# Optimization experiments

Hardware: AMD Instinct MI355X
Metric: run time of the kernel (lower is better)

## Reference

```python
import jax, jax.numpy as jnp
import numpy as np
from jax import lax

EPS = 1e-5
SLOPE = 0.01  # LeakyReLU negative slope
MAX_DISP = 5
KSIZE = 3  # correlation patch kernel size


def conv_bn_lrelu(x, w, b, g, be, stride=1):
    # x: (B, Cin, L), w: (Cout, Cin, K)
    k = w.shape[-1]
    pad = (k - 1) // 2
    y = lax.conv_general_dilated(x, w, (stride,), [(pad, pad)],
                                 dimension_numbers=('NCH', 'OIH', 'NCH'))
    y = y + b[None, :, None]
    # BatchNorm1d in training mode: biased batch stats over (B, L)
    m = y.mean(axis=(0, 2), keepdims=True)
    v = y.var(axis=(0, 2), keepdims=True)
    y = g[None, :, None] * (y - m) * lax.rsqrt(v + EPS) + be[None, :, None]
    return jnp.where(y >= 0, y, SLOPE * y)


def upsample_nearest(x, size):
    # F.interpolate(mode='nearest'): idx = floor(i * L_in / L_out)
    L = x.shape[-1]
    idx = (jnp.arange(size) * L) // size
    return x[:, :, idx]


def fusion(f1, f2, K=KSIZE, D=MAX_DISP):
    # Banded correlation: corr[b, d, i] = <patch1[b,:,i], patch2[b,:,clamp(i+d)]>
    # where patches stack K clamped neighbors along the channel dim.
    B, C, N = f1.shape
    h = K // 2
    win = jnp.clip(jnp.arange(N)[:, None] + jnp.arange(-h, h + 1)[None, :], 0, N - 1)  # (N, K)
    p1 = f1[:, :, win].transpose(0, 1, 3, 2).reshape(B, C * K, N)
    p2 = f2[:, :, win].transpose(0, 1, 3, 2).reshape(B, C * K, N)
    pts = jnp.arange(N)
    bands = []
    for d in range(-D, D + 1):  # small fixed loop over 2D+1 = 11 displacements
        j = jnp.clip(pts + d, 0, N - 1)
        bands.append(jnp.sum(p1 * p2[:, :, j], axis=1))  # (B, N)
    return jnp.stack(bands, axis=1)  # (B, 2D+1, N)


def _make_block(key, cin, cout, k):
    kw, _ = jax.random.split(key)
    scale = np.sqrt(2.0 / (1.0 + 0.1 ** 2) / (cin * k)).astype(np.float32)
    w = jax.random.normal(kw, (cout, cin, k), dtype=jnp.float32) * scale
    b = jnp.zeros((cout,), jnp.float32)
    g = jnp.ones((cout,), jnp.float32)
    be = jnp.zeros((cout,), jnp.float32)
    return w, b, g, be


def setup_inputs() -> dict:
    key = jax.random.key(0)
    ks = jax.random.split(key, 8)
    B, N, CIN = 8, 16384, 1
    scan1 = jax.random.normal(ks[0], (B, N, CIN), dtype=jnp.float32)
    inp = {'scan1': scan1}
    specs = [('enc0', CIN, 64, 3), ('enc1', 64, 128, 3), ('enc2', 128, 256, 3),
             ('dec1', 2 * MAX_DISP + 1 + 128, 128, 3), ('dec0', 128 + 64, 128, 3),
             ('flow', 128 + CIN, 2, 1)]
    for i, (name, cin, cout, k) in enumerate(specs):
        w, b, g, be = _make_block(ks[i + 1], cin, cout, k)
        inp[name + '_w'] = w
        inp[name + '_b'] = b
        inp[name + '_g'] = g
        inp[name + '_be'] = be
    return inp


def reference(scan1,
              enc0_w, enc0_b, enc0_g, enc0_be,
              enc1_w, enc1_b, enc1_g, enc1_be,
              enc2_w, enc2_b, enc2_g, enc2_be,
              dec1_w, dec1_b, dec1_g, dec1_be,
              dec0_w, dec0_b, dec0_g, dec0_be,
              flow_w, flow_b, flow_g, flow_be):
    x1 = scan1.transpose(0, 2, 1)  # (B, Cin, N)
    # scan2 defaults to scan1, so feat2_* == feat1_* (identical BN batch stats)
    f0 = conv_bn_lrelu(x1, enc0_w, enc0_b, enc0_g, enc0_be, stride=2)
    f1 = conv_bn_lrelu(f0, enc1_w, enc1_b, enc1_g, enc1_be, stride=2)
    f2 = conv_bn_lrelu(f1, enc2_w, enc2_b, enc2_g, enc2_be, stride=2)
    feat = fusion(f2, f2)  # (B, 11, N/8)
    up1 = upsample_nearest(feat, f1.shape[-1])
    up1 = jnp.concatenate((f1, up1), axis=1)
    up1 = conv_bn_lrelu(up1, dec1_w, dec1_b, dec1_g, dec1_be, stride=1)
    up0 = upsample_nearest(up1, f0.shape[-1])
    up0 = jnp.concatenate((f0, up0), axis=1)
    up0 = conv_bn_lrelu(up0, dec0_w, dec0_b, dec0_g, dec0_be, stride=1)
    out = upsample_nearest(up0, x1.shape[-1])
    out = jnp.concatenate((x1, out), axis=1)
    out = conv_bn_lrelu(out, flow_w, flow_b, flow_g, flow_be, stride=1)
    return out.transpose(0, 2, 1)  # (B, N, 2)
```

## Files before the change

kernel.cpp:

```cpp
#include <hip/hip_runtime.h>
#include <cstddef>

#define SLOPE 0.01f
#define BN_EPS 1e-5f

typedef __attribute__((ext_vector_type(8))) short short8;
typedef __attribute__((ext_vector_type(4))) float floatx4;

__device__ __forceinline__ float lrelu(float t) { return fmaxf(t, SLOPE * t); }

__device__ __forceinline__ unsigned short f2bf(float f) {
    union { float f; unsigned int u; } x; x.f = f;
    unsigned int r = (x.u + 0x7fff + ((x.u >> 16) & 1)) >> 16;
    return (unsigned short)r;
}
__device__ __forceinline__ float bf2f(unsigned short h) {
    union { unsigned int u; float f; } x; x.u = ((unsigned int)h) << 16;
    return x.f;
}

__device__ __forceinline__ void bn_coeff(const float* __restrict__ st,
                                         const float* __restrict__ g,
                                         const float* __restrict__ be,
                                         float invN, int c, float& sc, float& sh) {
    float m   = st[c] * invN;
    float var = fmaf(st[256 + c], invN, -m * m);
    float r   = rsqrtf(var + BN_EPS);
    sc = g[c] * r;
    sh = fmaf(-sc, m, be[c]);
}

__device__ __forceinline__ void reorder1(const float* __restrict__ w,
                                         unsigned short* __restrict__ wr,
                                         int Cout, int Cinpad, int Cin, int id) {
    int ci = id % Cinpad;
    int rest = id / Cinpad;
    int co = rest % Cout;
    int t  = rest / Cout;
    float v = (ci < Cin) ? w[((size_t)co * Cin + ci) * 3 + t] : 0.0f;
    wr[id] = f2bf(v);
}

__global__ __launch_bounds__(256) void prepw_all_kernel(
    const float* __restrict__ w1, unsigned short* __restrict__ o1,
    const float* __restrict__ w2, unsigned short* __restrict__ o2,
    const float* __restrict__ w3, unsigned short* __restrict__ o3,
    const float* __restrict__ w4, unsigned short* __restrict__ o4)
{
    int id = blockIdx.x * 256 + threadIdx.x;
    const int n1 = 3 * 128 * 64;
    const int n2 = 3 * 256 * 128;
    const int n3 = 3 * 128 * 160;
    const int n4 = 3 * 128 * 192;
    if (id < n1) { reorder1(w1, o1, 128, 64, 64, id); return; }
    id -= n1;
    if (id < n2) { reorder1(w2, o2, 256, 128, 128, id); return; }
    id -= n2;
    if (id < n3) { reorder1(w3, o3, 128, 160, 139, id); return; }
    id -= n3;
    if (id < n4) { reorder1(w4, o4, 128, 192, 192, id); return; }
}

__global__ __launch_bounds__(256) void enc0_kernel(
    const float* __restrict__ x, const float* __restrict__ w,
    const float* __restrict__ bias, unsigned short* __restrict__ f0,
    float* __restrict__ st)
{
    __shared__ float ssum[64], ssq[64];
    const int tid = threadIdx.x;
    const int co  = tid & 63;
    const int b   = blockIdx.z;
    if (tid < 64) { ssum[tid] = 0.f; ssq[tid] = 0.f; }
    __syncthreads();
    const float w0 = w[co * 3], w1 = w[co * 3 + 1], w2 = w[co * 3 + 2];
    const float bs = bias[co];
    const float* xb = x + (size_t)b * 16384;
    float lsum = 0.f, lsq = 0.f;
    const int obase = blockIdx.x * 128 + (tid >> 6) * 32;
    for (int k = 0; k < 32; ++k) {
        int o = obase + k;
        int xi = 2 * o - 1;
        float x0v = (xi >= 0) ? xb[xi] : 0.f;
        float a = bs;
        a = fmaf(w0, x0v, a);
        a = fmaf(w1, xb[xi + 1], a);
        a = fmaf(w2, xb[xi + 2], a);
        f0[((size_t)(b * 8192 + o)) * 64 + co] = f2bf(a);
        lsum += a; lsq = fmaf(a, a, lsq);
    }
    atomicAdd(&ssum[co], lsum);
    atomicAdd(&ssq[co], lsq);
    __syncthreads();
    if (tid < 64) {
        atomicAdd(&st[tid],       ssum[tid]);
        atomicAdd(&st[256 + tid], ssq[tid]);
    }
}

template<int STRIDE>
__global__ __launch_bounds__(256) void conv_mfma_kernel(
    const unsigned short* __restrict__ xA, int CAc,
    const float* __restrict__ stA, const float* __restrict__ gA,
    const float* __restrict__ beA, float invNA,
    const unsigned short* __restrict__ xB, int CBc,
    const float* __restrict__ stB, const float* __restrict__ gB,
    const float* __restrict__ beB, float invNB,
    const unsigned short* __restrict__ Wr, const float* __restrict__ bias,
    unsigned short* __restrict__ out, int L_in, int L_out, int Cout,
    float* __restrict__ st)
{
    constexpr int SEG = 127 * STRIDE + 3;
    __shared__ __align__(16) unsigned short x_tile[2][SEG * 32];
    __shared__ float ssum[64], ssq[64];
    __shared__ float csc[192], csh[192];

    const int tid  = threadIdx.x;
    const int wv   = tid >> 6;
    const int lane = tid & 63;
    const int col  = lane & 15;
    const int quad = lane >> 4;
    const int oblk = blockIdx.x * 128;
    const int cob  = blockIdx.y * 64;
    const int b    = blockIdx.z;
    const int nch    = CAc + CBc;
    const int CApad  = CAc * 32;
    const int CBpad  = CBc * 32;
    const int Cinpad = nch * 32;
    const int LB     = L_in >> 1;
    const bool nA = (stA != nullptr);
    const bool nB = (stB != nullptr);

    if (tid < 64) { ssum[tid] = 0.f; ssq[tid] = 0.f; }
    for (int c = tid; c < Cinpad; c += 256) {
        float sc = 1.f, sh = 0.f;
        if (c < CApad) { if (nA) bn_coeff(stA, gA, beA, invNA, c, sc, sh); }
        else           { if (nB) bn_coeff(stB, gB, beB, invNB, c - CApad, sc, sh); }
        csc[c] = sc; csh[c] = sh;
    }

    floatx4 acc[2][4];
    #pragma unroll
    for (int ps = 0; ps < 2; ++ps)
        #pragma unroll
        for (int s = 0; s < 4; ++s)
            acc[ps][s] = (floatx4){0.f, 0.f, 0.f, 0.f};

    const int x0 = oblk * STRIDE - 1;

    auto stage = [&](int ch, int buf) {
        const bool applyN = (ch < CAc) ? nA : nB;
        for (int r = tid; r < SEG * 4; r += 256) {
            const int pi = r >> 2, part = r & 3;
            const int gp = x0 + pi;
            short8 v = {0, 0, 0, 0, 0, 0, 0, 0};
            if (gp >= 0 && gp < L_in) {
                if (ch < CAc)
                    v = *(const short8*)(xA + ((size_t)b * L_in + gp) * CApad + ch * 32 + part * 8);
                else
                    v = *(const short8*)(xB + ((size_t)b * LB + (gp >> 1)) * CBpad + (ch - CAc) * 32 + part * 8);
                if (applyN) {
                    const int cb = ch * 32 + part * 8;
                    #pragma unroll
                    for (int e = 0; e < 8; ++e) {
                        float f = bf2f((unsigned short)v[e]);
                        f = lrelu(fmaf(f, csc[cb + e], csh[cb + e]));
                        v[e] = (short)f2bf(f);
                    }
                }
            }
            *(short8*)(x_tile[buf] + (size_t)r * 8) = v;
        }
    };

    __syncthreads();
    stage(0, 0);
    __syncthreads();

    for (int ch = 0; ch < nch; ++ch) {
        const int cur = ch & 1;
        if (ch + 1 < nch) stage(ch + 1, cur ^ 1);

        #pragma unroll
        for (int t = 0; t < 3; ++t) {
            short8 bfr[4];
            #pragma unroll
            for (int s = 0; s < 4; ++s)
                bfr[s] = *(const short8*)(Wr +
                    ((size_t)(t * Cout + cob + s * 16 + col)) * Cinpad + ch * 32 + quad * 8);
            #pragma unroll
            for (int ps = 0; ps < 2; ++ps) {
                const int xi = (wv * 32 + ps * 16 + col) * STRIDE + t;
                short8 afr = *(const short8*)(x_tile[cur] + xi * 32 + quad * 8);
                #pragma unroll
                for (int s = 0; s < 4; ++s)
                    acc[ps][s] = __builtin_amdgcn_mfma_f32_16x16x32_bf16(afr, bfr[s], acc[ps][s], 0, 0, 0);
            }
        }
        __syncthreads();
    }

    float bv[4];
    #pragma unroll
    for (int s = 0; s < 4; ++s) bv[s] = bias[cob + s * 16 + col];
    #pragma unroll
    for (int ps = 0; ps < 2; ++ps)
        #pragma unroll
        for (int s = 0; s < 4; ++s)
            #pragma unroll
            for (int r = 0; r < 4; ++r)
                acc[ps][s][r] += bv[s];

    #pragma unroll
    for (int ps = 0; ps < 2; ++ps) {
        const int pos0 = oblk + wv * 32 + ps * 16 + quad * 4;
        #pragma unroll
        for (int s = 0; s < 4; ++s) {
            unsigned short* op = out + ((size_t)b * L_out + pos0) * Cout + cob + s * 16 + col;
            #pragma unroll
            for (int r = 0; r < 4; ++r)
                op[(size_t)r * Cout] = f2bf(acc[ps][s][r]);
        }
    }

    #pragma unroll
    for (int s = 0; s < 4; ++s) {
        float v = 0.f, q = 0.f;
        #pragma unroll
        for (int ps = 0; ps < 2; ++ps)
            #pragma unroll
            for (int r = 0; r < 4; ++r) {
                float a = acc[ps][s][r];
                v += a; q = fmaf(a, a, q);
            }
        v += __shfl_xor(v, 16); v += __shfl_xor(v, 32);
        q += __shfl_xor(q, 16); q += __shfl_xor(q, 32);
        if (quad == 0) {
            atomicAdd(&ssum[s * 16 + col], v);
            atomicAdd(&ssq[s * 16 + col],  q);
        }
    }
    __syncthreads();
    if (tid < 64) {
        atomicAdd(&st[cob + tid],       ssum[tid]);
        atomicAdd(&st[256 + cob + tid], ssq[tid]);
    }
}

__global__ __launch_bounds__(256) void fusion_kernel(
    const unsigned short* __restrict__ f2,
    const float* __restrict__ st, const float* __restrict__ g,
    const float* __restrict__ be, float invN,
    unsigned short* __restrict__ feat)
{
    constexpr int ROWS = 44;
    constexpr int CPAD = 272;
    __shared__ __align__(16) unsigned short tile[ROWS * CPAD];
    __shared__ float csc[256], csh[256];
    const int tid = threadIdx.x;
    const int p0  = blockIdx.x * 32;
    const int b   = blockIdx.y;
    const unsigned short* base = f2 + (size_t)b * 2048 * 256;

    {
        float sc, sh;
        bn_coeff(st, g, be, invN, tid, sc, sh);
        csc[tid] = sc; csh[tid] = sh;
    }
    __syncthreads();
    float scr[8], shr[8];
    {
        const int cb = (tid & 31) * 8;
        #pragma unroll
        for (int e = 0; e < 8; ++e) { scr[e] = csc[cb + e]; shr[e] = csh[cb + e]; }
    }
    for (int r = tid; r < ROWS * 32; r += 256) {
        int row = r >> 5, piece = r & 31;
        int grow = min(max(p0 - 6 + row, 0), 2047);
        short8 v = *(const short8*)(base + (size_t)grow * 256 + piece * 8);
        #pragma unroll
        for (int e = 0; e < 8; ++e) {
            float f = bf2f((unsigned short)v[e]);
            f = lrelu(fmaf(f, scr[e], shr[e]));
            v[e] = (short)f2bf(f);
        }
        *(short8*)(tile + row * CPAD + piece * 8) = v;
    }
    __syncthreads();

    const int il = tid >> 3;
    const int q  = tid & 7;
    const int i  = p0 + il;

    float acc[11];
    #pragma unroll
    for (int d = 0; d < 11; ++d) acc[d] = 0.f;

    int ra[3];
    #pragma unroll
    for (int j = 0; j < 3; ++j)
        ra[j] = (min(max(i + j - 1, 0), 2047) - p0 + 6) * CPAD;
    int rb[11][3];
    #pragma unroll
    for (int d = 0; d < 11; ++d) {
        int i2 = min(max(i + d - 5, 0), 2047);
        #pragma unroll
        for (int j = 0; j < 3; ++j)
            rb[d][j] = (min(max(i2 + j - 1, 0), 2047) - p0 + 6) * CPAD;
    }

    for (int ck = 0; ck < 4; ++ck) {
        const int coff = q * 32 + ck * 8;
        float fa[3][8];
        #pragma unroll
        for (int j = 0; j < 3; ++j) {
            short8 v = *(const short8*)(tile + ra[j] + coff);
            #pragma unroll
            for (int e = 0; e < 8; ++e) fa[j][e] = bf2f((unsigned short)v[e]);
        }
        #pragma unroll
        for (int d = 0; d < 11; ++d) {
            #pragma unroll
            for (int j = 0; j < 3; ++j) {
                short8 v = *(const short8*)(tile + rb[d][j] + coff);
                #pragma unroll
                for (int e = 0; e < 8; ++e)
                    acc[d] = fmaf(fa[j][e], bf2f((unsigned short)v[e]), acc[d]);
            }
        }
    }

    #pragma unroll
    for (int d = 0; d < 11; ++d) {
        acc[d] += __shfl_xor(acc[d], 1);
        acc[d] += __shfl_xor(acc[d], 2);
        acc[d] += __shfl_xor(acc[d], 4);
    }
    if (q == 0) {
        unsigned short* op = feat + ((size_t)(b * 2048 + i)) * 32;
        #pragma unroll
        for (int d = 0; d < 11; ++d) op[d] = f2bf(acc[d]);
        #pragma unroll
        for (int d = 11; d < 32; ++d) op[d] = 0;
    }
}

__global__ __launch_bounds__(256) void flow_kernel(
    const float* __restrict__ scan1, const unsigned short* __restrict__ d0,
    const float* __restrict__ st4, const float* __restrict__ g4,
    const float* __restrict__ be4, float invN4,
    const float* __restrict__ fw, const float* __restrict__ fb,
    float* __restrict__ outr, float* __restrict__ st)
{
    __shared__ float s4[4][4];
    __shared__ float csc[128], csh[128];
    const int tid = threadIdx.x;
    const int b = blockIdx.z;
    const int i = blockIdx.x * 256 + tid;
    if (tid < 128) {
        float sc, sh;
        bn_coeff(st4, g4, be4, invN4, tid, sc, sh);
        csc[tid] = sc; csh[tid] = sh;
    }
    __syncthreads();
    float sv = scan1[(size_t)b * 16384 + i];
    const unsigned short* row = d0 + ((size_t)(b * 8192 + (i >> 1))) * 128;
    float a0 = fmaf(fw[0],   sv, fb[0]);
    float a1 = fmaf(fw[129], sv, fb[1]);
    for (int c8 = 0; c8 < 16; ++c8) {
        short8 v = *(const short8*)(row + c8 * 8);
        #pragma unroll
        for (int j = 0; j < 8; ++j) {
            int cc = c8 * 8 + j;
            float f = bf2f((unsigned short)v[j]);
            f = lrelu(fmaf(f, csc[cc], csh[cc]));
            a0 = fmaf(fw[1 + cc],   f, a0);
            a1 = fmaf(fw[130 + cc], f, a1);
        }
    }
    float2 o; o.x = a0; o.y = a1;
    *(float2*)(outr + ((size_t)(b * 16384 + i)) * 2) = o;
    float s0 = a0, q0 = a0 * a0, s1 = a1, q1 = a1 * a1;
    #pragma unroll
    for (int off = 1; off < 64; off <<= 1) {
        s0 += __shfl_xor(s0, off); q0 += __shfl_xor(q0, off);
        s1 += __shfl_xor(s1, off); q1 += __shfl_xor(q1, off);
    }
    if ((tid & 63) == 0) {
        int w = tid >> 6;
        s4[w][0] = s0; s4[w][1] = q0; s4[w][2] = s1; s4[w][3] = q1;
    }
    __syncthreads();
    if (tid == 0) {
        float t0 = 0, t1 = 0, t2 = 0, t3 = 0;
        for (int w = 0; w < 4; ++w) {
            t0 += s4[w][0]; t1 += s4[w][1]; t2 += s4[w][2]; t3 += s4[w][3];
        }
        atomicAdd(&st[0],   t0); atomicAdd(&st[256],     t1);
        atomicAdd(&st[1],   t2); atomicAdd(&st[256 + 1], t3);
    }
}

__global__ __launch_bounds__(256) void final_kernel(
    const float* __restrict__ raw, const float* __restrict__ st,
    const float* __restrict__ g, const float* __restrict__ be,
    float invN, float* __restrict__ out)
{
    int idx = blockIdx.x * 256 + threadIdx.x;
    float sc0, sh0, sc1, sh1;
    bn_coeff(st, g, be, invN, 0, sc0, sh0);
    bn_coeff(st, g, be, invN, 1, sc1, sh1);
    float2 v = *(const float2*)(raw + (size_t)idx * 2);
    float2 o;
    o.x = lrelu(fmaf(v.x, sc0, sh0));
    o.y = lrelu(fmaf(v.y, sc1, sh1));
    *(float2*)(out + (size_t)idx * 2) = o;
}


extern "C" void kernel_launch(void* const* d_in, const int* in_sizes, int n_in,
                              void* d_out, int out_size, void* d_ws, size_t ws_size,
                              hipStream_t stream)
{
    const int B = 8;
    const float* scan1 = (const float*)d_in[0];
    const float* enc0_w = (const float*)d_in[1];
    const float* enc0_b = (const float*)d_in[2];
    const float* enc0_g = (const float*)d_in[3];
    const float* enc0_be= (const float*)d_in[4];
    const float* enc1_w = (const float*)d_in[5];
    const float* enc1_b = (const float*)d_in[6];
    const float* enc1_g = (const float*)d_in[7];
    const float* enc1_be= (const float*)d_in[8];
    const float* enc2_w = (const float*)d_in[9];
    const float* enc2_b = (const float*)d_in[10];
    const float* enc2_g = (const float*)d_in[11];
    const float* enc2_be= (const float*)d_in[12];
    const float* dec1_w = (const float*)d_in[13];
    const float* dec1_b = (const float*)d_in[14];
    const float* dec1_g = (const float*)d_in[15];
    const float* dec1_be= (const float*)d_in[16];
    const float* dec0_w = (const float*)d_in[17];
    const float* dec0_b = (const float*)d_in[18];
    const float* dec0_g = (const float*)d_in[19];
    const float* dec0_be= (const float*)d_in[20];
    const float* flow_w = (const float*)d_in[21];
    const float* flow_b = (const float*)d_in[22];
    const float* flow_g = (const float*)d_in[23];
    const float* flow_be= (const float*)d_in[24];

    char* ws = (char*)d_ws;
    unsigned short* f0    = (unsigned short*)(ws);
    unsigned short* f1    = (unsigned short*)(ws + 8388608);
    unsigned short* f2    = (unsigned short*)(ws + 16777216);
    unsigned short* featn = (unsigned short*)(ws + 25165824);
    unsigned short* d1    = (unsigned short*)(ws + 26214400);
    unsigned short* d0    = (unsigned short*)(ws + 34603008);
    float*  flow_r = (float*)(ws + 51380224);
    unsigned short* wr1 = (unsigned short*)(ws + 52428800);
    unsigned short* wr2 = (unsigned short*)(ws + 52477952);
    unsigned short* wr3 = (unsigned short*)(ws + 52674560);
    unsigned short* wr4 = (unsigned short*)(ws + 52797440);
    float* st = (float*)(ws + 52944896);
    float* st0 = st, *st1 = st + 512, *st2 = st + 1024;
    float* st3 = st + 1536, *st4 = st + 2048, *st5 = st + 2560;

    const float iN0 = 1.0f / (B * 8192.0f);
    const float iN1 = 1.0f / (B * 4096.0f);
    const float iN2 = 1.0f / (B * 2048.0f);
    const float iN3 = 1.0f / (B * 4096.0f);
    const float iN4 = 1.0f / (B * 8192.0f);
    const float iN5 = 1.0f / (B * 16384.0f);

    hipMemsetAsync(st, 0, 6 * 512 * sizeof(float), stream);

    prepw_all_kernel<<<1008, 256, 0, stream>>>(enc1_w, wr1, enc2_w, wr2,
                                               dec1_w, wr3, dec0_w, wr4);

    enc0_kernel<<<dim3(64, 1, B), 256, 0, stream>>>(scan1, enc0_w, enc0_b, f0, st0);

    conv_mfma_kernel<2><<<dim3(32, 2, B), 256, 0, stream>>>(
        f0, 2, st0, enc0_g, enc0_be, iN0,
        nullptr, 0, nullptr, nullptr, nullptr, 0.f,
        wr1, enc1_b, f1, 8192, 4096, 128, st1);

    conv_mfma_kernel<2><<<dim3(16, 4, B), 256, 0, stream>>>(
        f1, 4, st1, enc1_g, enc1_be, iN1,
        nullptr, 0, nullptr, nullptr, nullptr, 0.f,
        wr2, enc2_b, f2, 4096, 2048, 256, st2);

    fusion_kernel<<<dim3(64, B), 256, 0, stream>>>(f2, st2, enc2_g, enc2_be, iN2, featn);

    conv_mfma_kernel<1><<<dim3(32, 2, B), 256, 0, stream>>>(
        f1, 4, st1, enc1_g, enc1_be, iN1,
        featn, 1, nullptr, nullptr, nullptr, 0.f,
        wr3, dec1_b, d1, 4096, 4096, 128, st3);

    conv_mfma_kernel<1><<<dim3(64, 2, B), 256, 0, stream>>>(
        f0, 2, st0, enc0_g, enc0_be, iN0,
        d1, 4, st3, dec1_g, dec1_be, iN3,
        wr4, dec0_b, d0, 8192, 8192, 128, st4);

    flow_kernel<<<dim3(64, 1, B), 256, 0, stream>>>(
        scan1, d0, st4, dec0_g, dec0_be, iN4, flow_w, flow_b, flow_r, st5);

    final_kernel<<<512, 256, 0, stream>>>(flow_r, st5, flow_g, flow_be, iN5, (float*)d_out);
}
```

Baseline: 285.1 us.

## Stage weights in LDS with register prefetch and padded tile stride

The conv MFMA kernel now loads the next channel's input and weight slices into registers before the MFMA loop and writes them to double-buffered LDS after it. This lets global load latency overlap with compute. Weights are now shared from LDS across waves instead of each wave reading them from global memory. Both tiles use a padded row stride of 36 elements to reduce LDS bank conflicts. In exchange the kernel uses more LDS and registers, which may lower occupancy.

```diff
diff --git a/kernel.cpp b/kernel.cpp
--- a/kernel.cpp
+++ b/kernel.cpp
@@ -109,8 +109,11 @@
     unsigned short* __restrict__ out, int L_in, int L_out, int Cout,
     float* __restrict__ st)
 {
-    constexpr int SEG = 127 * STRIDE + 3;
-    __shared__ __align__(16) unsigned short x_tile[2][SEG * 32];
+    constexpr int SEG  = 127 * STRIDE + 3;
+    constexpr int XPC  = (SEG * 4 + 255) / 256;
+    constexpr int XPAD = 36;
+    __shared__ __align__(16) unsigned short x_tile[2][SEG * XPAD];
+    __shared__ __align__(16) unsigned short w_tile[2][3 * 64 * XPAD];
     __shared__ float ssum[64], ssq[64];
     __shared__ float csc[192], csh[192];
 
@@ -147,18 +150,46 @@
 
     const int x0 = oblk * STRIDE - 1;
 
-    auto stage = [&](int ch, int buf) {
+    short8 xr[XPC];
+    short8 wr3[3];
+
+    auto load_regs = [&](int ch) {
+        #pragma unroll
+        for (int k = 0; k < XPC; ++k) {
+            const int r = tid + k * 256;
+            short8 v = {0, 0, 0, 0, 0, 0, 0, 0};
+            if (r < SEG * 4) {
+                const int pi = r >> 2, part = r & 3;
+                const int gp = x0 + pi;
+                if (gp >= 0 && gp < L_in) {
+                    if (ch < CAc)
+                        v = *(const short8*)(xA + ((size_t)b * L_in + gp) * CApad + ch * 32 + part * 8);
+                    else
+                        v = *(const short8*)(xB + ((size_t)b * LB + (gp >> 1)) * CBpad + (ch - CAc) * 32 + part * 8);
+                }
+            }
+            xr[k] = v;
+        }
+        #pragma unroll
+        for (int k = 0; k < 3; ++k) {
+            const int r = tid + k * 256;
+            const int part = r & 3;
+            const int co   = (r >> 2) & 63;
+            const int t    = r >> 8;
+            wr3[k] = *(const short8*)(Wr + ((size_t)(t * Cout + cob + co)) * Cinpad + ch * 32 + part * 8);
+        }
+    };
+
+    auto write_regs = [&](int ch, int buf) {
         const bool applyN = (ch < CAc) ? nA : nB;
-        for (int r = tid; r < SEG * 4; r += 256) {
-            const int pi = r >> 2, part = r & 3;
-            const int gp = x0 + pi;
-            short8 v = {0, 0, 0, 0, 0, 0, 0, 0};
-            if (gp >= 0 && gp < L_in) {
-                if (ch < CAc)
-                    v = *(const short8*)(xA + ((size_t)b * L_in + gp) * CApad + ch * 32 + part * 8);
-                else
-                    v = *(const short8*)(xB + ((size_t)b * LB + (gp >> 1)) * CBpad + (ch - CAc) * 32 + part * 8);
-                if (applyN) {
+        #pragma unroll
+        for (int k = 0; k < XPC; ++k) {
+            const int r = tid + k * 256;
+            if (r < SEG * 4) {
+                const int pi = r >> 2, part = r & 3;
+                const int gp = x0 + pi;
+                short8 v = xr[k];
+                if (applyN && gp >= 0 && gp < L_in) {
                     const int cb = ch * 32 + part * 8;
                     #pragma unroll
                     for (int e = 0; e < 8; ++e) {
@@ -167,35 +198,44 @@
                         v[e] = (short)f2bf(f);
                     }
                 }
+                *(short8*)(x_tile[buf] + pi * XPAD + part * 8) = v;
             }
-            *(short8*)(x_tile[buf] + (size_t)r * 8) = v;
+        }
+        #pragma unroll
+        for (int k = 0; k < 3; ++k) {
+            const int r = tid + k * 256;
+            const int part = r & 3;
+            const int co   = (r >> 2) & 63;
+            const int t    = r >> 8;
+            *(short8*)(w_tile[buf] + (t * 64 + co) * XPAD + part * 8) = wr3[k];
         }
     };
 
-    __syncthreads();
-    stage(0, 0);
+    load_regs(0);
+    __syncthreads();
+    write_regs(0, 0);
     __syncthreads();
 
     for (int ch = 0; ch < nch; ++ch) {
         const int cur = ch & 1;
-        if (ch + 1 < nch) stage(ch + 1, cur ^ 1);
+        if (ch + 1 < nch) load_regs(ch + 1);
 
         #pragma unroll
         for (int t = 0; t < 3; ++t) {
             short8 bfr[4];
             #pragma unroll
             for (int s = 0; s < 4; ++s)
-                bfr[s] = *(const short8*)(Wr +
-                    ((size_t)(t * Cout + cob + s * 16 + col)) * Cinpad + ch * 32 + quad * 8);
+                bfr[s] = *(const short8*)(w_tile[cur] + (t * 64 + s * 16 + col) * XPAD + quad * 8);
             #pragma unroll
             for (int ps = 0; ps < 2; ++ps) {
                 const int xi = (wv * 32 + ps * 16 + col) * STRIDE + t;
-                short8 afr = *(const short8*)(x_tile[cur] + xi * 32 + quad * 8);
+                short8 afr = *(const short8*)(x_tile[cur] + xi * XPAD + quad * 8);
                 #pragma unroll
                 for (int s = 0; s < 4; ++s)
                     acc[ps][s] = __builtin_amdgcn_mfma_f32_16x16x32_bf16(afr, bfr[s], acc[ps][s], 0, 0, 0);
             }
         }
+        if (ch + 1 < nch) write_regs(ch + 1, cur ^ 1);
         __syncthreads();
     }
 
```

Result: faster. 252.5 us (-11.4%).
